# Kernel tuning notes

Hardware: AMD Instinct MI355X
Metric: run time of the kernel (lower is better)

## Reference

```python
import jax, jax.numpy as jnp
import numpy as np

WIDTH = 8  # fixed-point fractional bits (init arg Width)


def quantizer(x, width=WIDTH):
    # Fixed-point quantization to `width` fractional bits, clipped to [-1, 1].
    scale = jnp.asarray(2.0 ** width, x.dtype)
    return jnp.clip(jnp.round(x * scale) / scale, -1.0, 1.0)


def setup_inputs() -> dict:
    key = jax.random.key(0)
    k1, k2, k3 = jax.random.split(key, 3)
    N, H, W, C = 32, 56, 56, 128
    KH, KW, F = 3, 3, 256
    OH, OW = H - KH + 1, W - KW + 1  # valid padding, stride 1
    x = jax.random.normal(k1, (N, H, W, C), dtype=jnp.float32) * 0.5
    kernels = jax.random.normal(k2, (KH, KW, C, F), dtype=jnp.float32) * 0.01
    bias = jax.random.normal(k3, (OH, OW, F), dtype=jnp.float32) * 0.01
    return {"x": x, "kernels": kernels, "bias": bias}


def reference(x, kernels, bias):
    # Method == 'Fixed': quantize input and kernels, valid conv, quantize output,
    # then per-position bias add + ReLU.
    xq = quantizer(x)
    wq = quantizer(kernels)
    out = jax.lax.conv_general_dilated(
        xq, wq,
        window_strides=(1, 1),
        padding="VALID",
        dimension_numbers=("NHWC", "HWIO", "NHWC"),
    )
    out = quantizer(out)
    return jax.nn.relu(out + bias[None, :, :, :])
```

## Files before the change

kernel.cpp:

```cpp
#include <hip/hip_runtime.h>
#include <hip/hip_bf16.h>
#include <stdint.h>
#include <stddef.h>


typedef float  f32x4  __attribute__((ext_vector_type(4)));
typedef short  bf16x8 __attribute__((ext_vector_type(8)));

#define N_IMG 32
#define H_IN 56
#define W_IN 56
#define C_IN 128
#define F_OUT 256
#define OHW 54
#define M_TOTAL (N_IMG * OHW * OHW)
#define BM 128
#define BN 128
#define BK 64

__device__ __forceinline__ unsigned short quant_to_bf16(float x) {
    float a = rintf(x * 256.0f);
    a = fminf(fmaxf(a, -256.0f), 256.0f);
    float q = a * 0.00390625f;
    union { float f; unsigned int u; } cv; cv.f = q;
    return (unsigned short)(cv.u >> 16);
}

__device__ __forceinline__ void async_copy16(const unsigned short* g, unsigned short* l) {
    __builtin_amdgcn_global_load_lds(
        (const __attribute__((address_space(1))) unsigned int*)g,
        (__attribute__((address_space(3))) unsigned int*)l, 16, 0, 0);
}

__global__ __launch_bounds__(256) void quant_x_kernel(
        const float* __restrict__ x, unsigned short* __restrict__ xq) {
    int i = (blockIdx.x * 256 + threadIdx.x) * 4;
    float4 v = *reinterpret_cast<const float4*>(x + i);
    ushort4 o;
    o.x = quant_to_bf16(v.x);
    o.y = quant_to_bf16(v.y);
    o.z = quant_to_bf16(v.z);
    o.w = quant_to_bf16(v.w);
    *reinterpret_cast<ushort4*>(xq + i) = o;
}

__global__ __launch_bounds__(256) void quant_w_kernel(
        const float* __restrict__ w, unsigned short* __restrict__ wpf) {
    int idx = blockIdx.x * 256 + threadIdx.x;
    int j  = idx & 7;
    int l  = (idx >> 3) & 63;
    int g  = (idx >> 9) & 15;
    int ks = (idx >> 13) & 1;
    int hf = (idx >> 14) & 1;
    int kk = idx >> 15;
    int f  = g * 16 + (l & 15);
    int c  = hf * 64 + ks * 32 + (l >> 4) * 8 + j;
    wpf[idx] = quant_to_bf16(w[(kk * C_IN + c) * F_OUT + f]);
}

__global__ __launch_bounds__(256, 2) void conv_kernel(
        const unsigned short* __restrict__ xq,
        const unsigned short* __restrict__ wpf,
        const float* __restrict__ bias,
        float* __restrict__ out)
{
    __shared__ __attribute__((aligned(16))) unsigned short Alds[2][BM * BK];

    const int tid  = threadIdx.x;
    const int wave = tid >> 6;
    const int lane = tid & 63;
    const int bid  = blockIdx.x;
    const int mb   = bid >> 1;
    const int nb   = bid & 1;
    const int m0   = mb * BM;
    const int wr   = wave >> 1;
    const int wc   = wave & 1;

    const int row0 = tid >> 3;
    const int sw   = (tid & 7) ^ (row0 & 7);
    const int dstc = (tid & ~63) * 8;

    const unsigned short* a_base[4];
#pragma unroll
    for (int r = 0; r < 4; ++r) {
        int m = m0 + row0 + 32 * r;
        int n_img = m / (OHW * OHW);
        int rem   = m % (OHW * OHW);
        int oh = rem / OHW, ow = rem % OHW;
        a_base[r] = xq + (size_t)((n_img * H_IN + oh) * W_IN + ow) * C_IN + sw * 8;
    }

    auto stageA = [&](int t, unsigned short* Ab) {
        int kk = t >> 1, hf = t & 1;
        int kh = (kk * 43) >> 7, kw = kk - 3 * kh;
        int aoff = (kh * W_IN + kw) * C_IN + hf * 64;
#pragma unroll
        for (int r = 0; r < 4; ++r)
            async_copy16(a_base[r] + aoff, Ab + r * 2048 + dstc);
    };

    const unsigned short* b_base = wpf + (size_t)(nb * 8 + wc * 4) * 512 + lane * 8;

    bf16x8 bregA[4][2], bregB[4][2];
    auto loadB_A = [&](int t) {
#pragma unroll
        for (int ni = 0; ni < 4; ++ni)
#pragma unroll
            for (int ks = 0; ks < 2; ++ks)
                bregA[ni][ks] = *reinterpret_cast<const bf16x8*>(
                    b_base + t * 16384 + ks * 8192 + ni * 512);
    };
    auto loadB_B = [&](int t) {
#pragma unroll
        for (int ni = 0; ni < 4; ++ni)
#pragma unroll
            for (int ks = 0; ks < 2; ++ks)
                bregB[ni][ks] = *reinterpret_cast<const bf16x8*>(
                    b_base + t * 16384 + ks * 8192 + ni * 512);
    };

    const int mr = lane & 15;
    const int lq = lane >> 4;

    f32x4 acc[4][4];
#pragma unroll
    for (int i = 0; i < 4; ++i)
#pragma unroll
        for (int j = 0; j < 4; ++j) acc[i][j] = (f32x4)(0.0f);

    auto computeA = [&](const unsigned short* Ab) {
#pragma unroll
        for (int ks = 0; ks < 2; ++ks) {
            const int ch = (((ks * 4 + lq) ^ (mr & 7)) * 8);
            bf16x8 af[4];
#pragma unroll
            for (int mi = 0; mi < 4; ++mi)
                af[mi] = *reinterpret_cast<const bf16x8*>(
                    Ab + (wr * 64 + mi * 16 + mr) * BK + ch);
#pragma unroll
            for (int mi = 0; mi < 4; ++mi)
#pragma unroll
                for (int ni = 0; ni < 4; ++ni)
                    acc[mi][ni] = __builtin_amdgcn_mfma_f32_16x16x32_bf16(
                        af[mi], bregA[ni][ks], acc[mi][ni], 0, 0, 0);
        }
    };
    auto computeB = [&](const unsigned short* Ab) {
#pragma unroll
        for (int ks = 0; ks < 2; ++ks) {
            const int ch = (((ks * 4 + lq) ^ (mr & 7)) * 8);
            bf16x8 af[4];
#pragma unroll
            for (int mi = 0; mi < 4; ++mi)
                af[mi] = *reinterpret_cast<const bf16x8*>(
                    Ab + (wr * 64 + mi * 16 + mr) * BK + ch);
#pragma unroll
            for (int mi = 0; mi < 4; ++mi)
#pragma unroll
                for (int ni = 0; ni < 4; ++ni)
                    acc[mi][ni] = __builtin_amdgcn_mfma_f32_16x16x32_bf16(
                        af[mi], bregB[ni][ks], acc[mi][ni], 0, 0, 0);
        }
    };

    stageA(0, Alds[0]);
    loadB_A(0);
    __syncthreads();

#pragma unroll 1
    for (int tp = 0; tp < 8; ++tp) {
        stageA(2 * tp + 1, Alds[1]);
        loadB_B(2 * tp + 1);
        computeA(Alds[0]);
        __syncthreads();
        stageA(2 * tp + 2, Alds[0]);
        loadB_A(2 * tp + 2);
        computeB(Alds[1]);
        __syncthreads();
    }
    stageA(17, Alds[1]);
    loadB_B(17);
    computeA(Alds[0]);
    __syncthreads();
    computeB(Alds[1]);

    const int fcol0 = nb * BN + wc * 64 + mr;
#pragma unroll
    for (int mi = 0; mi < 4; ++mi) {
#pragma unroll
        for (int rr = 0; rr < 4; ++rr) {
            const int m = m0 + wr * 64 + mi * 16 + lq * 4 + rr;
            const float* brow = bias + (size_t)(m % (OHW * OHW)) * F_OUT;
            float* orow = out + (size_t)m * F_OUT;
#pragma unroll
            for (int ni = 0; ni < 4; ++ni) {
                float v = acc[mi][ni][rr];
                float t = rintf(v * 256.0f);
                t = fminf(fmaxf(t, -256.0f), 256.0f);
                float o = t * 0.00390625f + brow[fcol0 + ni * 16];
                orow[fcol0 + ni * 16] = fmaxf(o, 0.0f);
            }
        }
    }
}

extern "C" void kernel_launch(void* const* d_in, const int* in_sizes, int n_in,
                              void* d_out, int out_size, void* d_ws, size_t ws_size,
                              hipStream_t stream) {
    (void)in_sizes; (void)n_in; (void)out_size;
    const float* x    = (const float*)d_in[0];
    const float* w    = (const float*)d_in[1];
    const float* bias = (const float*)d_in[2];
    float* out        = (float*)d_out;

    const size_t x_elems = (size_t)N_IMG * H_IN * W_IN * C_IN;
    const size_t w_elems = (size_t)9 * F_OUT * C_IN;
    const size_t xq_bytes = x_elems * sizeof(unsigned short);
    const size_t need = xq_bytes + w_elems * sizeof(unsigned short);
    if (ws_size < need) return;

    unsigned short* xq  = (unsigned short*)d_ws;
    unsigned short* wpf = (unsigned short*)((char*)d_ws + xq_bytes);

    quant_x_kernel<<<(int)(x_elems / (256 * 4)), 256, 0, stream>>>(x, xq);
    quant_w_kernel<<<(int)(w_elems / 256), 256, 0, stream>>>(w, wpf);
    conv_kernel<<<(M_TOTAL / BM) * 2, 256, 0, stream>>>(xq, wpf, bias, out);
}
```

Measured before the change: 86.85 us.

## Triple-buffer A tiles with fine-grained vmcnt waits and XCD-aware block remap

Switches the A-tile LDS staging from double to triple buffering so global-to-LDS copies run two iterations ahead, replacing full __syncthreads with s_waitcnt vmcnt(4) plus a raw barrier so the most recent copy stays in flight. Also remaps block indices so each XCD processes a contiguous range of output tiles, improving L2 reuse of overlapping input windows and weights. Costs extra LDS (48KB per block) and relies on exact hand-counted vmcnt accounting, which is fragile if the compiler reorders or adds memory ops.

```diff
diff --git a/kernel.cpp b/kernel.cpp
--- a/kernel.cpp
+++ b/kernel.cpp
@@ -64,17 +64,23 @@
         const float* __restrict__ bias,
         float* __restrict__ out)
 {
-    __shared__ __attribute__((aligned(16))) unsigned short Alds[2][BM * BK];
+    __shared__ __attribute__((aligned(16))) unsigned short Alds[3][BM * BK];
 
     const int tid  = threadIdx.x;
     const int wave = tid >> 6;
     const int lane = tid & 63;
-    const int bid  = blockIdx.x;
-    const int mb   = bid >> 1;
-    const int nb   = bid & 1;
-    const int m0   = mb * BM;
-    const int wr   = wave >> 1;
-    const int wc   = wave & 1;
+
+    int L;
+    {
+        int bid = blockIdx.x;
+        int xcd = bid & 7, idx = bid >> 3;
+        L = (xcd < 2) ? xcd * 183 + idx : 366 + (xcd - 2) * 182 + idx;
+    }
+    const int mb = L >> 1;
+    const int nb = L & 1;
+    const int m0 = mb * BM;
+    const int wr = wave >> 1;
+    const int wc = wave & 1;
 
     const int row0 = tid >> 3;
     const int sw   = (tid & 7) ^ (row0 & 7);
@@ -165,24 +171,40 @@
 
     stageA(0, Alds[0]);
     loadB_A(0);
-    __syncthreads();
-
-#pragma unroll 1
-    for (int tp = 0; tp < 8; ++tp) {
-        stageA(2 * tp + 1, Alds[1]);
-        loadB_B(2 * tp + 1);
-        computeA(Alds[0]);
-        __syncthreads();
-        stageA(2 * tp + 2, Alds[0]);
-        loadB_A(2 * tp + 2);
-        computeB(Alds[1]);
-        __syncthreads();
-    }
-    stageA(17, Alds[1]);
+    stageA(1, Alds[1]);
+    asm volatile("s_waitcnt vmcnt(4)" ::: "memory");
+    __builtin_amdgcn_s_barrier();
+
+#define STEP(T, CUR, NXT, LB, CP)                                   \
+    LB(T + 1);                                                      \
+    stageA(T + 2, Alds[NXT]);                                       \
+    CP(Alds[CUR]);                                                  \
+    asm volatile("s_waitcnt vmcnt(4)" ::: "memory");                \
+    __builtin_amdgcn_s_barrier();
+
+    STEP(0, 0, 2, loadB_B, computeA)
+    STEP(1, 1, 0, loadB_A, computeB)
+    STEP(2, 2, 1, loadB_B, computeA)
+    STEP(3, 0, 2, loadB_A, computeB)
+    STEP(4, 1, 0, loadB_B, computeA)
+    STEP(5, 2, 1, loadB_A, computeB)
+    STEP(6, 0, 2, loadB_B, computeA)
+    STEP(7, 1, 0, loadB_A, computeB)
+    STEP(8, 2, 1, loadB_B, computeA)
+    STEP(9, 0, 2, loadB_A, computeB)
+    STEP(10, 1, 0, loadB_B, computeA)
+    STEP(11, 2, 1, loadB_A, computeB)
+    STEP(12, 0, 2, loadB_B, computeA)
+    STEP(13, 1, 0, loadB_A, computeB)
+    STEP(14, 2, 1, loadB_B, computeA)
+    STEP(15, 0, 2, loadB_A, computeB)
+#undef STEP
+
     loadB_B(17);
-    computeA(Alds[0]);
-    __syncthreads();
-    computeB(Alds[1]);
+    computeA(Alds[1]);
+    asm volatile("s_waitcnt vmcnt(0)" ::: "memory");
+    __builtin_amdgcn_s_barrier();
+    computeB(Alds[2]);
 
     const int fcol0 = nb * BN + wc * 64 + mr;
 #pragma unroll
```

Result: slower. 101.8 us (+17.2%).

## Single-buffer B registers, raise occupancy, and remap blocks across XCDs

Applied to the files above, without the earlier changes.

B fragments are now held in one register set, loaded after each compute step instead of being double-buffered, so register use falls and launch bounds can target 4 blocks per CU. Block IDs are also remapped so that consecutive logical tiles, which share M rows and overlapping input windows, land on the same XCD for better L2 reuse. The cost is that B global-load latency is no longer hidden behind compute: the load issues after the MFMAs and must complete before the next compute, relying on the extra resident waves to cover the stall.

```diff
diff --git a/kernel.cpp b/kernel.cpp
--- a/kernel.cpp
+++ b/kernel.cpp
@@ -58,7 +58,7 @@
     wpf[idx] = quant_to_bf16(w[(kk * C_IN + c) * F_OUT + f]);
 }
 
-__global__ __launch_bounds__(256, 2) void conv_kernel(
+__global__ __launch_bounds__(256, 4) void conv_kernel(
         const unsigned short* __restrict__ xq,
         const unsigned short* __restrict__ wpf,
         const float* __restrict__ bias,
@@ -69,12 +69,18 @@
     const int tid  = threadIdx.x;
     const int wave = tid >> 6;
     const int lane = tid & 63;
-    const int bid  = blockIdx.x;
-    const int mb   = bid >> 1;
-    const int nb   = bid & 1;
-    const int m0   = mb * BM;
-    const int wr   = wave >> 1;
-    const int wc   = wave & 1;
+
+    int L;
+    {
+        int bid = blockIdx.x;
+        int xcd = bid & 7, idx = bid >> 3;
+        L = (xcd < 2) ? xcd * 183 + idx : 366 + (xcd - 2) * 182 + idx;
+    }
+    const int mb = L >> 1;
+    const int nb = L & 1;
+    const int m0 = mb * BM;
+    const int wr = wave >> 1;
+    const int wc = wave & 1;
 
     const int row0 = tid >> 3;
     const int sw   = (tid & 7) ^ (row0 & 7);
@@ -101,23 +107,15 @@
 
     const unsigned short* b_base = wpf + (size_t)(nb * 8 + wc * 4) * 512 + lane * 8;
 
-    bf16x8 bregA[4][2], bregB[4][2];
-    auto loadB_A = [&](int t) {
+    bf16x8 breg[4][2];
+    auto loadB = [&](int t) {
 #pragma unroll
         for (int ni = 0; ni < 4; ++ni)
 #pragma unroll
             for (int ks = 0; ks < 2; ++ks)
-                bregA[ni][ks] = *reinterpret_cast<const bf16x8*>(
+                breg[ni][ks] = *reinterpret_cast<const bf16x8*>(
                     b_base + t * 16384 + ks * 8192 + ni * 512);
     };
-    auto loadB_B = [&](int t) {
-#pragma unroll
-        for (int ni = 0; ni < 4; ++ni)
-#pragma unroll
-            for (int ks = 0; ks < 2; ++ks)
-                bregB[ni][ks] = *reinterpret_cast<const bf16x8*>(
-                    b_base + t * 16384 + ks * 8192 + ni * 512);
-    };
 
     const int mr = lane & 15;
     const int lq = lane >> 4;
@@ -128,7 +126,7 @@
 #pragma unroll
         for (int j = 0; j < 4; ++j) acc[i][j] = (f32x4)(0.0f);
 
-    auto computeA = [&](const unsigned short* Ab) {
+    auto compute = [&](const unsigned short* Ab) {
 #pragma unroll
         for (int ks = 0; ks < 2; ++ks) {
             const int ch = (((ks * 4 + lq) ^ (mr & 7)) * 8);
@@ -142,47 +140,30 @@
 #pragma unroll
                 for (int ni = 0; ni < 4; ++ni)
                     acc[mi][ni] = __builtin_amdgcn_mfma_f32_16x16x32_bf16(
-                        af[mi], bregA[ni][ks], acc[mi][ni], 0, 0, 0);
+                        af[mi], breg[ni][ks], acc[mi][ni], 0, 0, 0);
         }
     };
-    auto computeB = [&](const unsigned short* Ab) {
-#pragma unroll
-        for (int ks = 0; ks < 2; ++ks) {
-            const int ch = (((ks * 4 + lq) ^ (mr & 7)) * 8);
-            bf16x8 af[4];
-#pragma unroll
-            for (int mi = 0; mi < 4; ++mi)
-                af[mi] = *reinterpret_cast<const bf16x8*>(
-                    Ab + (wr * 64 + mi * 16 + mr) * BK + ch);
-#pragma unroll
-            for (int mi = 0; mi < 4; ++mi)
-#pragma unroll
-                for (int ni = 0; ni < 4; ++ni)
-                    acc[mi][ni] = __builtin_amdgcn_mfma_f32_16x16x32_bf16(
-                        af[mi], bregB[ni][ks], acc[mi][ni], 0, 0, 0);
-        }
-    };
 
     stageA(0, Alds[0]);
-    loadB_A(0);
+    loadB(0);
     __syncthreads();
 
 #pragma unroll 1
     for (int tp = 0; tp < 8; ++tp) {
         stageA(2 * tp + 1, Alds[1]);
-        loadB_B(2 * tp + 1);
-        computeA(Alds[0]);
+        compute(Alds[0]);
+        loadB(2 * tp + 1);
         __syncthreads();
         stageA(2 * tp + 2, Alds[0]);
-        loadB_A(2 * tp + 2);
-        computeB(Alds[1]);
+        compute(Alds[1]);
+        loadB(2 * tp + 2);
         __syncthreads();
     }
     stageA(17, Alds[1]);
-    loadB_B(17);
-    computeA(Alds[0]);
+    compute(Alds[0]);
+    loadB(17);
     __syncthreads();
-    computeB(Alds[1]);
+    compute(Alds[1]);
 
     const int fcol0 = nb * BN + wc * 64 + mr;
 #pragma unroll
```

Measured after the change: 151.8 us. +74.8%, slower.
